# Optimization experiments

Hardware: AMD Instinct MI355X
Metric: run time of the kernel (lower is better)

The kernel has to match this reference:

```python
import jax, jax.numpy as jnp
import numpy as np

NUM_EXPERTS = 8
TOP_K = 2
DIM = 1024
HIDDEN = 4096
B, S = 2, 1024


def setup_inputs() -> dict:
    key = jax.random.key(0)
    k_x, k_g, k_1, k_2, k_3 = jax.random.split(key, 5)
    s_d = 1.0 / np.sqrt(DIM)
    s_h = 1.0 / np.sqrt(HIDDEN)
    return {
        "x": jax.random.normal(k_x, (B, S, DIM), dtype=jnp.float32),
        "gate_w": jax.random.normal(k_g, (NUM_EXPERTS, DIM), dtype=jnp.float32) * s_d,
        "w1": jax.random.normal(k_1, (NUM_EXPERTS, HIDDEN, DIM), dtype=jnp.float32) * s_d,
        "w2": jax.random.normal(k_2, (NUM_EXPERTS, DIM, HIDDEN), dtype=jnp.float32) * s_h,
        "w3": jax.random.normal(k_3, (NUM_EXPERTS, HIDDEN, DIM), dtype=jnp.float32) * s_d,
    }


def reference(x, gate_w, w1, w2, w3):
    orig_shape = x.shape
    xt = x.reshape(-1, orig_shape[-1])                      # [T, D]
    scores = xt @ gate_w.T                                  # [T, E] (gate_softmax=False)
    top_vals, top_idx = jax.lax.top_k(scores, TOP_K)        # [T, K]
    top_w = jax.nn.softmax(top_vals, axis=-1)               # [T, K]
    # per-token combine weights over experts: [T, E]
    combine = jnp.einsum("tke,tk->te", jax.nn.one_hot(top_idx, NUM_EXPERTS, dtype=xt.dtype), top_w)
    # dense per-expert SwiGLU FFN; combine masks out unrouted experts
    h = jax.nn.silu(jnp.einsum("td,ehd->eth", xt, w1)) * jnp.einsum("td,ehd->eth", xt, w3)
    ye = jnp.einsum("eth,edh->etd", h, w2)                  # [E, T, D]
    y = jnp.einsum("te,etd->td", combine, ye)               # [T, D]
    return y.reshape(orig_shape)
```

## Files before the change

### kernel.cpp

```cpp
#include <hip/hip_runtime.h>
#include <hip/hip_bf16.h>

#define NUM_EXPERTS 8
#define TOPK 2
#define DIM 1024
#define HIDDEN 4096
#define T_TOKENS 2048
#define TOTAL_ROWS (T_TOKENS * TOPK)
#define LDSP 40

typedef __bf16 bf16x8 __attribute__((ext_vector_type(8)));
typedef float f32x4 __attribute__((ext_vector_type(4)));

__device__ __forceinline__ unsigned short f2bf(float f) {
  unsigned int u = __float_as_uint(f);
  u += 0x7FFF + ((u >> 16) & 1);
  return (unsigned short)(u >> 16);
}

__device__ __forceinline__ void gl_lds16(const void* g, void* l) {
  __builtin_amdgcn_global_load_lds(
      (const __attribute__((address_space(1))) unsigned int*)g,
      (__attribute__((address_space(3))) unsigned int*)l, 16, 0, 0);
}

__global__ __launch_bounds__(256) void cast_kernel(
    const float* __restrict__ src, unsigned short* __restrict__ dst, int n8) {
  int i = blockIdx.x * blockDim.x + threadIdx.x;
  int stride = gridDim.x * blockDim.x;
  for (; i < n8; i += stride) {
    float4 a = ((const float4*)src)[i * 2];
    float4 b = ((const float4*)src)[i * 2 + 1];
    ushort4 o0, o1;
    o0.x = f2bf(a.x); o0.y = f2bf(a.y); o0.z = f2bf(a.z); o0.w = f2bf(a.w);
    o1.x = f2bf(b.x); o1.y = f2bf(b.y); o1.z = f2bf(b.z); o1.w = f2bf(b.w);
    ((ushort4*)dst)[i * 2] = o0;
    ((ushort4*)dst)[i * 2 + 1] = o1;
  }
}

__global__ __launch_bounds__(256) void gate_kernel(
    const float* __restrict__ x, const float* __restrict__ gw,
    int* __restrict__ tok_idx, float* __restrict__ tok_w) {
  int wid = threadIdx.x >> 6;
  int lane = threadIdx.x & 63;
  int t = blockIdx.x * 4 + wid;
  if (t >= T_TOKENS) return;

  float xv[16];
#pragma unroll
  for (int i = 0; i < 16; i++) xv[i] = x[t * DIM + lane + i * 64];

  float s[NUM_EXPERTS];
#pragma unroll
  for (int e = 0; e < NUM_EXPERTS; e++) {
    float acc = 0.f;
#pragma unroll
    for (int i = 0; i < 16; i++) acc += xv[i] * gw[e * DIM + lane + i * 64];
#pragma unroll
    for (int off = 32; off; off >>= 1) acc += __shfl_xor(acc, off, 64);
    s[e] = acc;
  }
  if (lane == 0) {
    int i0 = 0;
    float v0 = s[0];
#pragma unroll
    for (int e = 1; e < NUM_EXPERTS; e++)
      if (s[e] > v0) { v0 = s[e]; i0 = e; }
    int i1 = -1;
    float v1 = -1e30f;
#pragma unroll
    for (int e = 0; e < NUM_EXPERTS; e++)
      if (e != i0 && s[e] > v1) { v1 = s[e]; i1 = e; }
    float e1 = __expf(v1 - v0);
    float d = 1.f + e1;
    tok_idx[t * 2] = i0;
    tok_idx[t * 2 + 1] = i1;
    tok_w[t * 2] = 1.f / d;
    tok_w[t * 2 + 1] = e1 / d;
  }
}

__global__ void scatter_kernel(const int* __restrict__ tok_idx,
                               const float* __restrict__ tok_w,
                               int* __restrict__ row_token,
                               float* __restrict__ row_weight,
                               int* __restrict__ counts,
                               int* __restrict__ offsets) {
  __shared__ int sc[NUM_EXPERTS];
  int tid = threadIdx.x;
  if (tid < NUM_EXPERTS) sc[tid] = 0;
  __syncthreads();
  for (int i = tid; i < TOTAL_ROWS; i += blockDim.x)
    atomicAdd(&sc[tok_idx[i]], 1);
  __syncthreads();
  if (tid == 0) {
    int run = 0;
    for (int e = 0; e < NUM_EXPERTS; e++) {
      int c = sc[e];
      counts[e] = c;
      offsets[e] = run;
      sc[e] = run;
      run += c;
    }
  }
  __syncthreads();
  for (int i = tid; i < TOTAL_ROWS; i += blockDim.x) {
    int e = tok_idx[i];
    int pos = atomicAdd(&sc[e], 1);
    row_token[pos] = i >> 1;
    row_weight[pos] = tok_w[i];
  }
}


__global__ __launch_bounds__(256) void ffn1_fast(
    const unsigned short* __restrict__ xb, const unsigned short* __restrict__ w1b,
    const unsigned short* __restrict__ w3b, const int* __restrict__ row_token,
    const int* __restrict__ counts, const int* __restrict__ offsets,
    unsigned short* __restrict__ hbuf) {
  int e = blockIdx.z;
  int cnt = counts[e];
  int m0 = blockIdx.y * 128;
  if (m0 >= cnt) return;
  int n0 = blockIdx.x * 128;
  int row_base = offsets[e];

  __shared__ __align__(16) unsigned short lA[128 * 32];
  __shared__ __align__(16) unsigned short lB1[128 * 32];
  __shared__ __align__(16) unsigned short lB3[128 * 32];

  int tid = threadIdx.x;
  int lane = tid & 63, wid = tid >> 6;
  int quad = lane >> 4, l16 = lane & 15;
  int wm = wid >> 1, wn = wid & 1;

  long aoff[2];
#pragma unroll
  for (int it = 0; it < 2; it++) {
    int c = it * 256 + tid;
    int r = c >> 2, seg = c & 3;
    int t = (m0 + r) < cnt ? row_token[row_base + m0 + r] : 0;
    aoff[it] = (long)t * DIM + seg * 8;
  }
  const unsigned short* w1p = w1b + (long)e * HIDDEN * DIM + (long)n0 * DIM;
  const unsigned short* w3p = w3b + (long)e * HIDDEN * DIM + (long)n0 * DIM;

  f32x4 acc1[4][4], acc3[4][4];
#pragma unroll
  for (int mi = 0; mi < 4; mi++)
#pragma unroll
    for (int ni = 0; ni < 4; ni++) {
      acc1[mi][ni] = (f32x4){0.f, 0.f, 0.f, 0.f};
      acc3[mi][ni] = (f32x4){0.f, 0.f, 0.f, 0.f};
    }

  for (int k0 = 0; k0 < DIM; k0 += 32) {
#pragma unroll
    for (int it = 0; it < 2; it++) {
      int c = it * 256 + tid;
      long boff = (long)(c >> 2) * DIM + (c & 3) * 8 + k0;
      gl_lds16(xb + aoff[it] + k0, &lA[c * 8]);
      gl_lds16(w1p + boff, &lB1[c * 8]);
      gl_lds16(w3p + boff, &lB3[c * 8]);
    }
    __syncthreads();

    bf16x8 af[4], b1f[4], b3f[4];
#pragma unroll
    for (int i = 0; i < 4; i++) {
      af[i]  = *(const bf16x8*)(const void*)&lA[(wm * 64 + i * 16 + l16) * 32 + quad * 8];
      b1f[i] = *(const bf16x8*)(const void*)&lB1[(wn * 64 + i * 16 + l16) * 32 + quad * 8];
      b3f[i] = *(const bf16x8*)(const void*)&lB3[(wn * 64 + i * 16 + l16) * 32 + quad * 8];
    }
#pragma unroll
    for (int mi = 0; mi < 4; mi++)
#pragma unroll
      for (int ni = 0; ni < 4; ni++) {
        acc1[mi][ni] = __builtin_amdgcn_mfma_f32_16x16x32_bf16(af[mi], b1f[ni], acc1[mi][ni], 0, 0, 0);
        acc3[mi][ni] = __builtin_amdgcn_mfma_f32_16x16x32_bf16(af[mi], b3f[ni], acc3[mi][ni], 0, 0, 0);
      }
    __syncthreads();
  }

#pragma unroll
  for (int mi = 0; mi < 4; mi++) {
#pragma unroll
    for (int r = 0; r < 4; r++) {
      int m = wm * 64 + mi * 16 + quad * 4 + r;
      if (m0 + m < cnt) {
        long rowoff = (long)(row_base + m0 + m) * HIDDEN;
#pragma unroll
        for (int ni = 0; ni < 4; ni++) {
          int n = n0 + wn * 64 + ni * 16 + l16;
          float v1 = acc1[mi][ni][r];
          float v3 = acc3[mi][ni][r];
          float sig = 1.f / (1.f + __expf(-v1));
          hbuf[rowoff + n] = f2bf(v1 * sig * v3);
        }
      }
    }
  }
}

__global__ __launch_bounds__(256) void ffn2_fast(
    const unsigned short* __restrict__ hbuf, const unsigned short* __restrict__ w2b,
    const int* __restrict__ row_token, const float* __restrict__ row_weight,
    const int* __restrict__ counts, const int* __restrict__ offsets,
    float* __restrict__ y) {
  int e = blockIdx.z;
  int cnt = counts[e];
  int m0 = blockIdx.y * 64;
  if (m0 >= cnt) return;
  int n0 = blockIdx.x * 128;
  int row_base = offsets[e];

  __shared__ __align__(16) unsigned short lA[64 * 32];
  __shared__ __align__(16) unsigned short lB[128 * 32];

  int tid = threadIdx.x;
  int lane = tid & 63, wid = tid >> 6;
  int quad = lane >> 4, l16 = lane & 15;
  int wm = wid >> 1, wn = wid & 1;

  int ar = tid >> 2, aseg = tid & 3;
  int arow = (m0 + ar) < cnt ? (row_base + m0 + ar) : row_base;
  long aoff = (long)arow * HIDDEN + aseg * 8;

  const unsigned short* w2p = w2b + (long)e * DIM * HIDDEN + (long)n0 * HIDDEN;

  f32x4 acc[2][4];
#pragma unroll
  for (int mi = 0; mi < 2; mi++)
#pragma unroll
    for (int ni = 0; ni < 4; ni++) acc[mi][ni] = (f32x4){0.f, 0.f, 0.f, 0.f};

  for (int k0 = 0; k0 < HIDDEN; k0 += 32) {
    gl_lds16(hbuf + aoff + k0, &lA[tid * 8]);
#pragma unroll
    for (int it = 0; it < 2; it++) {
      int c = it * 256 + tid;
      long boff = (long)(c >> 2) * HIDDEN + (c & 3) * 8 + k0;
      gl_lds16(w2p + boff, &lB[c * 8]);
    }
    __syncthreads();

    bf16x8 af[2], bf[4];
#pragma unroll
    for (int i = 0; i < 2; i++)
      af[i] = *(const bf16x8*)(const void*)&lA[(wm * 32 + i * 16 + l16) * 32 + quad * 8];
#pragma unroll
    for (int i = 0; i < 4; i++)
      bf[i] = *(const bf16x8*)(const void*)&lB[(wn * 64 + i * 16 + l16) * 32 + quad * 8];
#pragma unroll
    for (int mi = 0; mi < 2; mi++)
#pragma unroll
      for (int ni = 0; ni < 4; ni++)
        acc[mi][ni] = __builtin_amdgcn_mfma_f32_16x16x32_bf16(af[mi], bf[ni], acc[mi][ni], 0, 0, 0);
    __syncthreads();
  }

#pragma unroll
  for (int mi = 0; mi < 2; mi++) {
#pragma unroll
    for (int r = 0; r < 4; r++) {
      int m = wm * 32 + mi * 16 + quad * 4 + r;
      if (m0 + m < cnt) {
        int t = row_token[row_base + m0 + m];
        float wgt = row_weight[row_base + m0 + m];
        long yoff = (long)t * DIM + n0 + wn * 64;
#pragma unroll
        for (int ni = 0; ni < 4; ni++)
          atomicAdd(&y[yoff + ni * 16 + l16], wgt * acc[mi][ni][r]);
      }
    }
  }
}


__global__ __launch_bounds__(256) void ffn1_slow(
    const float* __restrict__ x, const float* __restrict__ w1,
    const float* __restrict__ w3, const int* __restrict__ row_token,
    const int* __restrict__ counts, const int* __restrict__ offsets,
    unsigned short* __restrict__ hbuf) {
  int e = blockIdx.z;
  int cnt = counts[e];
  int m0 = blockIdx.y * 128;
  if (m0 >= cnt) return;
  int n0 = blockIdx.x * 128;
  int row_base = offsets[e];

  __shared__ __align__(16) unsigned short lA[128 * LDSP];
  __shared__ __align__(16) unsigned short lB1[128 * LDSP];
  __shared__ __align__(16) unsigned short lB3[128 * LDSP];

  int tid = threadIdx.x;
  int lane = tid & 63, wid = tid >> 6;
  int quad = lane >> 4, l16 = lane & 15;
  int wm = wid >> 1, wn = wid & 1;

  long aoff[4];
  bool aval[4];
#pragma unroll
  for (int it = 0; it < 4; it++) {
    int linear = it * 256 + tid;
    int r = linear >> 3, c4 = linear & 7;
    bool v = (m0 + r) < cnt;
    aval[it] = v;
    int t = v ? row_token[row_base + m0 + r] : 0;
    aoff[it] = (long)t * DIM + c4 * 4;
  }
  const float* w1p = w1 + (long)e * HIDDEN * DIM;
  const float* w3p = w3 + (long)e * HIDDEN * DIM;

  f32x4 acc1[4][4], acc3[4][4];
#pragma unroll
  for (int mi = 0; mi < 4; mi++)
#pragma unroll
    for (int ni = 0; ni < 4; ni++) {
      acc1[mi][ni] = (f32x4){0.f, 0.f, 0.f, 0.f};
      acc3[mi][ni] = (f32x4){0.f, 0.f, 0.f, 0.f};
    }

  for (int k0 = 0; k0 < DIM; k0 += 32) {
#pragma unroll
    for (int it = 0; it < 4; it++) {
      int linear = it * 256 + tid;
      int r = linear >> 3, c4 = linear & 7;
      float4 v = make_float4(0.f, 0.f, 0.f, 0.f);
      if (aval[it]) v = *(const float4*)(x + aoff[it] + k0);
      ushort4 b;
      b.x = f2bf(v.x); b.y = f2bf(v.y); b.z = f2bf(v.z); b.w = f2bf(v.w);
      *(ushort4*)&lA[r * LDSP + c4 * 4] = b;
    }
#pragma unroll
    for (int it = 0; it < 4; it++) {
      int linear = it * 256 + tid;
      int r = linear >> 3, c4 = linear & 7;
      long boff = (long)(n0 + r) * DIM + k0 + c4 * 4;
      float4 v1 = *(const float4*)(w1p + boff);
      float4 v3 = *(const float4*)(w3p + boff);
      ushort4 b1, b3;
      b1.x = f2bf(v1.x); b1.y = f2bf(v1.y); b1.z = f2bf(v1.z); b1.w = f2bf(v1.w);
      b3.x = f2bf(v3.x); b3.y = f2bf(v3.y); b3.z = f2bf(v3.z); b3.w = f2bf(v3.w);
      *(ushort4*)&lB1[r * LDSP + c4 * 4] = b1;
      *(ushort4*)&lB3[r * LDSP + c4 * 4] = b3;
    }
    __syncthreads();

    bf16x8 af[4], b1f[4], b3f[4];
#pragma unroll
    for (int i = 0; i < 4; i++) {
      af[i]  = *(const bf16x8*)(const void*)&lA[(wm * 64 + i * 16 + l16) * LDSP + quad * 8];
      b1f[i] = *(const bf16x8*)(const void*)&lB1[(wn * 64 + i * 16 + l16) * LDSP + quad * 8];
      b3f[i] = *(const bf16x8*)(const void*)&lB3[(wn * 64 + i * 16 + l16) * LDSP + quad * 8];
    }
#pragma unroll
    for (int mi = 0; mi < 4; mi++)
#pragma unroll
      for (int ni = 0; ni < 4; ni++) {
        acc1[mi][ni] = __builtin_amdgcn_mfma_f32_16x16x32_bf16(af[mi], b1f[ni], acc1[mi][ni], 0, 0, 0);
        acc3[mi][ni] = __builtin_amdgcn_mfma_f32_16x16x32_bf16(af[mi], b3f[ni], acc3[mi][ni], 0, 0, 0);
      }
    __syncthreads();
  }

#pragma unroll
  for (int mi = 0; mi < 4; mi++) {
#pragma unroll
    for (int r = 0; r < 4; r++) {
      int m = wm * 64 + mi * 16 + quad * 4 + r;
      if (m0 + m < cnt) {
        long rowoff = (long)(row_base + m0 + m) * HIDDEN;
#pragma unroll
        for (int ni = 0; ni < 4; ni++) {
          int n = n0 + wn * 64 + ni * 16 + l16;
          float v1 = acc1[mi][ni][r];
          float v3 = acc3[mi][ni][r];
          float sig = 1.f / (1.f + __expf(-v1));
          hbuf[rowoff + n] = f2bf(v1 * sig * v3);
        }
      }
    }
  }
}

__global__ __launch_bounds__(256) void ffn2_slow(
    const unsigned short* __restrict__ hbuf, const float* __restrict__ w2,
    const int* __restrict__ row_token, const float* __restrict__ row_weight,
    const int* __restrict__ counts, const int* __restrict__ offsets,
    float* __restrict__ y) {
  int e = blockIdx.z;
  int cnt = counts[e];
  int m0 = blockIdx.y * 128;
  if (m0 >= cnt) return;
  int n0 = blockIdx.x * 128;
  int row_base = offsets[e];

  __shared__ __align__(16) unsigned short lA[128 * LDSP];
  __shared__ __align__(16) unsigned short lB[128 * LDSP];

  int tid = threadIdx.x;
  int lane = tid & 63, wid = tid >> 6;
  int quad = lane >> 4, l16 = lane & 15;
  int wm = wid >> 1, wn = wid & 1;

  const float* w2p = w2 + (long)e * DIM * HIDDEN;

  f32x4 acc[4][4];
#pragma unroll
  for (int mi = 0; mi < 4; mi++)
#pragma unroll
    for (int ni = 0; ni < 4; ni++) acc[mi][ni] = (f32x4){0.f, 0.f, 0.f, 0.f};

  for (int k0 = 0; k0 < HIDDEN; k0 += 32) {
#pragma unroll
    for (int it = 0; it < 2; it++) {
      int linear = it * 256 + tid;
      int r = linear >> 2, c8 = linear & 3;
      float4 v = make_float4(0.f, 0.f, 0.f, 0.f);
      if (m0 + r < cnt)
        v = *(const float4*)(hbuf + (long)(row_base + m0 + r) * HIDDEN + k0 + c8 * 8);
      *(float4*)&lA[r * LDSP + c8 * 8] = v;
    }
#pragma unroll
    for (int it = 0; it < 4; it++) {
      int linear = it * 256 + tid;
      int r = linear >> 3, c4 = linear & 7;
      float4 v = *(const float4*)(w2p + (long)(n0 + r) * HIDDEN + k0 + c4 * 4);
      ushort4 b;
      b.x = f2bf(v.x); b.y = f2bf(v.y); b.z = f2bf(v.z); b.w = f2bf(v.w);
      *(ushort4*)&lB[r * LDSP + c4 * 4] = b;
    }
    __syncthreads();

    bf16x8 af[4], bfr[4];
#pragma unroll
    for (int i = 0; i < 4; i++) {
      af[i]  = *(const bf16x8*)(const void*)&lA[(wm * 64 + i * 16 + l16) * LDSP + quad * 8];
      bfr[i] = *(const bf16x8*)(const void*)&lB[(wn * 64 + i * 16 + l16) * LDSP + quad * 8];
    }
#pragma unroll
    for (int mi = 0; mi < 4; mi++)
#pragma unroll
      for (int ni = 0; ni < 4; ni++)
        acc[mi][ni] = __builtin_amdgcn_mfma_f32_16x16x32_bf16(af[mi], bfr[ni], acc[mi][ni], 0, 0, 0);
    __syncthreads();
  }

#pragma unroll
  for (int mi = 0; mi < 4; mi++) {
#pragma unroll
    for (int r = 0; r < 4; r++) {
      int m = wm * 64 + mi * 16 + quad * 4 + r;
      if (m0 + m < cnt) {
        int t = row_token[row_base + m0 + m];
        float wgt = row_weight[row_base + m0 + m];
        long yoff = (long)t * DIM + n0 + wn * 64;
#pragma unroll
        for (int ni = 0; ni < 4; ni++)
          atomicAdd(&y[yoff + ni * 16 + l16], wgt * acc[mi][ni][r]);
      }
    }
  }
}

extern "C" void kernel_launch(void* const* d_in, const int* in_sizes, int n_in,
                              void* d_out, int out_size, void* d_ws, size_t ws_size,
                              hipStream_t stream) {
  const float* x = (const float*)d_in[0];
  const float* gw = (const float*)d_in[1];
  const float* w1 = (const float*)d_in[2];
  const float* w2 = (const float*)d_in[3];
  const float* w3 = (const float*)d_in[4];
  float* y = (float*)d_out;

  char* ws = (char*)d_ws;
  int* row_token = (int*)ws;
  float* row_weight = (float*)(ws + 16384);
  int* counts = (int*)(ws + 32768);
  int* offsets = (int*)(ws + 32768 + 32);
  int* tok_idx = (int*)(ws + 32896);
  float* tok_w = (float*)(ws + 32896 + 16384);
  const size_t HBUF_OFF = 65664;
  const size_t XB_OFF   = HBUF_OFF + 33554432ull;
  const size_t W1B_OFF  = XB_OFF + 4194304ull;
  const size_t W2B_OFF  = W1B_OFF + 67108864ull;
  const size_t W3B_OFF  = W2B_OFF + 67108864ull;
  const size_t NEED     = W3B_OFF + 67108864ull;
  unsigned short* hbuf = (unsigned short*)(ws + HBUF_OFF);

  hipMemsetAsync(d_out, 0, (size_t)T_TOKENS * DIM * sizeof(float), stream);
  gate_kernel<<<T_TOKENS / 4, 256, 0, stream>>>(x, gw, tok_idx, tok_w);
  scatter_kernel<<<1, 256, 0, stream>>>(tok_idx, tok_w, row_token, row_weight, counts, offsets);

  if (ws_size >= NEED) {
    unsigned short* xb  = (unsigned short*)(ws + XB_OFF);
    unsigned short* w1b = (unsigned short*)(ws + W1B_OFF);
    unsigned short* w2b = (unsigned short*)(ws + W2B_OFF);
    unsigned short* w3b = (unsigned short*)(ws + W3B_OFF);
    const int NW8 = NUM_EXPERTS * HIDDEN * DIM / 8;
    cast_kernel<<<512, 256, 0, stream>>>(x, xb, T_TOKENS * DIM / 8);
    cast_kernel<<<2048, 256, 0, stream>>>(w1, w1b, NW8);
    cast_kernel<<<2048, 256, 0, stream>>>(w3, w3b, NW8);
    cast_kernel<<<2048, 256, 0, stream>>>(w2, w2b, NW8);
    ffn1_fast<<<dim3(HIDDEN / 128, T_TOKENS / 128, NUM_EXPERTS), 256, 0, stream>>>(
        xb, w1b, w3b, row_token, counts, offsets, hbuf);
    ffn2_fast<<<dim3(DIM / 128, T_TOKENS / 64, NUM_EXPERTS), 256, 0, stream>>>(
        hbuf, w2b, row_token, row_weight, counts, offsets, y);
  } else {
    ffn1_slow<<<dim3(HIDDEN / 128, T_TOKENS / 128, NUM_EXPERTS), 256, 0, stream>>>(
        x, w1, w3, row_token, counts, offsets, hbuf);
    ffn2_slow<<<dim3(DIM / 128, T_TOKENS / 128, NUM_EXPERTS), 256, 0, stream>>>(
        hbuf, w2, row_token, row_weight, counts, offsets, y);
  }
}
```

Measured before the change: 759.6 us.

## Double-buffer LDS in FFN kernels, enlarge ffn2 tile with split-K, fix grid size

Both fast FFN GEMMs now use double-buffered LDS with async global-to-LDS prefetch of the next K slice, synchronised by explicit vmcnt waits and barriers, so loads overlap MFMA work. ffn2 moves from 64-row to 128-row tiles and splits the HIDDEN reduction into two halves that accumulate into the output with atomics. The grid y-dimension is raised to cover TOTAL_ROWS, so experts holding more than T_TOKENS/128 tiles of rows are no longer truncated. The cost is doubled LDS use and more atomic traffic.

```diff
diff --git a/kernel.cpp b/kernel.cpp
--- a/kernel.cpp
+++ b/kernel.cpp
@@ -23,6 +23,9 @@
       (const __attribute__((address_space(1))) unsigned int*)g,
       (__attribute__((address_space(3))) unsigned int*)l, 16, 0, 0);
 }
+
+#define WAIT_VM(N) __builtin_amdgcn_s_waitcnt(0x0F70 | (N))
+#define BARRIER() __builtin_amdgcn_s_barrier()
 
 __global__ __launch_bounds__(256) void cast_kernel(
     const float* __restrict__ src, unsigned short* __restrict__ dst, int n8) {
@@ -126,9 +129,9 @@
   int n0 = blockIdx.x * 128;
   int row_base = offsets[e];
 
-  __shared__ __align__(16) unsigned short lA[128 * 32];
-  __shared__ __align__(16) unsigned short lB1[128 * 32];
-  __shared__ __align__(16) unsigned short lB3[128 * 32];
+  __shared__ __align__(16) unsigned short lA[2][128 * 32];
+  __shared__ __align__(16) unsigned short lB1[2][128 * 32];
+  __shared__ __align__(16) unsigned short lB3[2][128 * 32];
 
   int tid = threadIdx.x;
   int lane = tid & 63, wid = tid >> 6;
@@ -136,12 +139,14 @@
   int wm = wid >> 1, wn = wid & 1;
 
   long aoff[2];
+  long boff[2];
 #pragma unroll
   for (int it = 0; it < 2; it++) {
     int c = it * 256 + tid;
     int r = c >> 2, seg = c & 3;
     int t = (m0 + r) < cnt ? row_token[row_base + m0 + r] : 0;
     aoff[it] = (long)t * DIM + seg * 8;
+    boff[it] = (long)r * DIM + seg * 8;
   }
   const unsigned short* w1p = w1b + (long)e * HIDDEN * DIM + (long)n0 * DIM;
   const unsigned short* w3p = w3b + (long)e * HIDDEN * DIM + (long)n0 * DIM;
@@ -155,23 +160,38 @@
       acc3[mi][ni] = (f32x4){0.f, 0.f, 0.f, 0.f};
     }
 
-  for (int k0 = 0; k0 < DIM; k0 += 32) {
-#pragma unroll
-    for (int it = 0; it < 2; it++) {
-      int c = it * 256 + tid;
-      long boff = (long)(c >> 2) * DIM + (c & 3) * 8 + k0;
-      gl_lds16(xb + aoff[it] + k0, &lA[c * 8]);
-      gl_lds16(w1p + boff, &lB1[c * 8]);
-      gl_lds16(w3p + boff, &lB3[c * 8]);
-    }
-    __syncthreads();
+#pragma unroll
+  for (int it = 0; it < 2; it++) {
+    int c = it * 256 + tid;
+    gl_lds16(xb + aoff[it], &lA[0][c * 8]);
+    gl_lds16(w1p + boff[it], &lB1[0][c * 8]);
+    gl_lds16(w3p + boff[it], &lB3[0][c * 8]);
+  }
+
+  int pc = 0;
+  for (int k0 = 0; k0 < DIM; k0 += 32, pc ^= 1) {
+    BARRIER();
+    if (k0 + 32 < DIM) {
+      int nb = pc ^ 1, kn = k0 + 32;
+#pragma unroll
+      for (int it = 0; it < 2; it++) {
+        int c = it * 256 + tid;
+        gl_lds16(xb + aoff[it] + kn, &lA[nb][c * 8]);
+        gl_lds16(w1p + boff[it] + kn, &lB1[nb][c * 8]);
+        gl_lds16(w3p + boff[it] + kn, &lB3[nb][c * 8]);
+      }
+      WAIT_VM(6);
+    } else {
+      WAIT_VM(0);
+    }
+    BARRIER();
 
     bf16x8 af[4], b1f[4], b3f[4];
 #pragma unroll
     for (int i = 0; i < 4; i++) {
-      af[i]  = *(const bf16x8*)(const void*)&lA[(wm * 64 + i * 16 + l16) * 32 + quad * 8];
-      b1f[i] = *(const bf16x8*)(const void*)&lB1[(wn * 64 + i * 16 + l16) * 32 + quad * 8];
-      b3f[i] = *(const bf16x8*)(const void*)&lB3[(wn * 64 + i * 16 + l16) * 32 + quad * 8];
+      af[i]  = *(const bf16x8*)(const void*)&lA[pc][(wm * 64 + i * 16 + l16) * 32 + quad * 8];
+      b1f[i] = *(const bf16x8*)(const void*)&lB1[pc][(wn * 64 + i * 16 + l16) * 32 + quad * 8];
+      b3f[i] = *(const bf16x8*)(const void*)&lB3[pc][(wn * 64 + i * 16 + l16) * 32 + quad * 8];
     }
 #pragma unroll
     for (int mi = 0; mi < 4; mi++)
@@ -180,7 +200,6 @@
         acc1[mi][ni] = __builtin_amdgcn_mfma_f32_16x16x32_bf16(af[mi], b1f[ni], acc1[mi][ni], 0, 0, 0);
         acc3[mi][ni] = __builtin_amdgcn_mfma_f32_16x16x32_bf16(af[mi], b3f[ni], acc3[mi][ni], 0, 0, 0);
       }
-    __syncthreads();
   }
 
 #pragma unroll
@@ -210,61 +229,81 @@
     float* __restrict__ y) {
   int e = blockIdx.z;
   int cnt = counts[e];
-  int m0 = blockIdx.y * 64;
+  int mt = blockIdx.y >> 1, kh = blockIdx.y & 1;
+  int m0 = mt * 128;
   if (m0 >= cnt) return;
   int n0 = blockIdx.x * 128;
   int row_base = offsets[e];
-
-  __shared__ __align__(16) unsigned short lA[64 * 32];
-  __shared__ __align__(16) unsigned short lB[128 * 32];
+  const int KHALF = HIDDEN / 2;
+  int kbeg = kh * KHALF;
+
+  __shared__ __align__(16) unsigned short lA[2][128 * 32];
+  __shared__ __align__(16) unsigned short lB[2][128 * 32];
 
   int tid = threadIdx.x;
   int lane = tid & 63, wid = tid >> 6;
   int quad = lane >> 4, l16 = lane & 15;
   int wm = wid >> 1, wn = wid & 1;
 
-  int ar = tid >> 2, aseg = tid & 3;
-  int arow = (m0 + ar) < cnt ? (row_base + m0 + ar) : row_base;
-  long aoff = (long)arow * HIDDEN + aseg * 8;
-
+  long aoff[2], boff[2];
+#pragma unroll
+  for (int it = 0; it < 2; it++) {
+    int c = it * 256 + tid;
+    int r = c >> 2, seg = c & 3;
+    int row = (m0 + r) < cnt ? (row_base + m0 + r) : row_base;
+    aoff[it] = (long)row * HIDDEN + seg * 8 + kbeg;
+    boff[it] = (long)r * HIDDEN + seg * 8 + kbeg;
+  }
   const unsigned short* w2p = w2b + (long)e * DIM * HIDDEN + (long)n0 * HIDDEN;
 
-  f32x4 acc[2][4];
-#pragma unroll
-  for (int mi = 0; mi < 2; mi++)
+  f32x4 acc[4][4];
+#pragma unroll
+  for (int mi = 0; mi < 4; mi++)
 #pragma unroll
     for (int ni = 0; ni < 4; ni++) acc[mi][ni] = (f32x4){0.f, 0.f, 0.f, 0.f};
 
-  for (int k0 = 0; k0 < HIDDEN; k0 += 32) {
-    gl_lds16(hbuf + aoff + k0, &lA[tid * 8]);
-#pragma unroll
-    for (int it = 0; it < 2; it++) {
-      int c = it * 256 + tid;
-      long boff = (long)(c >> 2) * HIDDEN + (c & 3) * 8 + k0;
-      gl_lds16(w2p + boff, &lB[c * 8]);
-    }
-    __syncthreads();
-
-    bf16x8 af[2], bf[4];
-#pragma unroll
-    for (int i = 0; i < 2; i++)
-      af[i] = *(const bf16x8*)(const void*)&lA[(wm * 32 + i * 16 + l16) * 32 + quad * 8];
-#pragma unroll
-    for (int i = 0; i < 4; i++)
-      bf[i] = *(const bf16x8*)(const void*)&lB[(wn * 64 + i * 16 + l16) * 32 + quad * 8];
-#pragma unroll
-    for (int mi = 0; mi < 2; mi++)
+#pragma unroll
+  for (int it = 0; it < 2; it++) {
+    int c = it * 256 + tid;
+    gl_lds16(hbuf + aoff[it], &lA[0][c * 8]);
+    gl_lds16(w2p + boff[it], &lB[0][c * 8]);
+  }
+
+  int pc = 0;
+  for (int k0 = 0; k0 < KHALF; k0 += 32, pc ^= 1) {
+    BARRIER();
+    if (k0 + 32 < KHALF) {
+      int nb = pc ^ 1, kn = k0 + 32;
+#pragma unroll
+      for (int it = 0; it < 2; it++) {
+        int c = it * 256 + tid;
+        gl_lds16(hbuf + aoff[it] + kn, &lA[nb][c * 8]);
+        gl_lds16(w2p + boff[it] + kn, &lB[nb][c * 8]);
+      }
+      WAIT_VM(4);
+    } else {
+      WAIT_VM(0);
+    }
+    BARRIER();
+
+    bf16x8 af[4], bfr[4];
+#pragma unroll
+    for (int i = 0; i < 4; i++) {
+      af[i]  = *(const bf16x8*)(const void*)&lA[pc][(wm * 64 + i * 16 + l16) * 32 + quad * 8];
+      bfr[i] = *(const bf16x8*)(const void*)&lB[pc][(wn * 64 + i * 16 + l16) * 32 + quad * 8];
+    }
+#pragma unroll
+    for (int mi = 0; mi < 4; mi++)
 #pragma unroll
       for (int ni = 0; ni < 4; ni++)
-        acc[mi][ni] = __builtin_amdgcn_mfma_f32_16x16x32_bf16(af[mi], bf[ni], acc[mi][ni], 0, 0, 0);
-    __syncthreads();
-  }
-
-#pragma unroll
-  for (int mi = 0; mi < 2; mi++) {
+        acc[mi][ni] = __builtin_amdgcn_mfma_f32_16x16x32_bf16(af[mi], bfr[ni], acc[mi][ni], 0, 0, 0);
+  }
+
+#pragma unroll
+  for (int mi = 0; mi < 4; mi++) {
 #pragma unroll
     for (int r = 0; r < 4; r++) {
-      int m = wm * 32 + mi * 16 + quad * 4 + r;
+      int m = wm * 64 + mi * 16 + quad * 4 + r;
       if (m0 + m < cnt) {
         int t = row_token[row_base + m0 + m];
         float wgt = row_weight[row_base + m0 + m];
@@ -504,14 +543,14 @@
     cast_kernel<<<2048, 256, 0, stream>>>(w1, w1b, NW8);
     cast_kernel<<<2048, 256, 0, stream>>>(w3, w3b, NW8);
     cast_kernel<<<2048, 256, 0, stream>>>(w2, w2b, NW8);
-    ffn1_fast<<<dim3(HIDDEN / 128, T_TOKENS / 128, NUM_EXPERTS), 256, 0, stream>>>(
+    ffn1_fast<<<dim3(HIDDEN / 128, TOTAL_ROWS / 128, NUM_EXPERTS), 256, 0, stream>>>(
         xb, w1b, w3b, row_token, counts, offsets, hbuf);
-    ffn2_fast<<<dim3(DIM / 128, T_TOKENS / 64, NUM_EXPERTS), 256, 0, stream>>>(
+    ffn2_fast<<<dim3(DIM / 128, (TOTAL_ROWS / 128) * 2, NUM_EXPERTS), 256, 0, stream>>>(
         hbuf, w2b, row_token, row_weight, counts, offsets, y);
   } else {
-    ffn1_slow<<<dim3(HIDDEN / 128, T_TOKENS / 128, NUM_EXPERTS), 256, 0, stream>>>(
+    ffn1_slow<<<dim3(HIDDEN / 128, TOTAL_ROWS / 128, NUM_EXPERTS), 256, 0, stream>>>(
         x, w1, w3, row_token, counts, offsets, hbuf);
-    ffn2_slow<<<dim3(DIM / 128, T_TOKENS / 128, NUM_EXPERTS), 256, 0, stream>>>(
+    ffn2_slow<<<dim3(DIM / 128, TOTAL_ROWS / 128, NUM_EXPERTS), 256, 0, stream>>>(
         hbuf, w2, row_token, row_weight, counts, offsets, y);
   }
 }
```

New measurement: 694.4 us. 1.09x faster.
